# Optimization experiments

Hardware: AMD Instinct MI355X
Metric: run time of the kernel (lower is better)

The kernel has to match this reference:

```python
import jax, jax.numpy as jnp
import numpy as np

N_NODES = 100000
N_EDGES = 1600000
N_FEAT = 16
HEADS = 4


def _feast_conv(x, src, dst, U, c, W, b):
    """FeaStConv: q = softmax_h(u^T(x_j - x_i) + c); out_i = mean_j sum_h q_h * (W_h x_j) + b."""
    n = x.shape[0]
    e = src.shape[0]
    xj = x[src]                                   # [E, Fin] gather
    q = jax.nn.softmax(jnp.matmul(xj - x[dst], U) + c, axis=-1)   # [E, H]
    xs = jnp.matmul(xj, W).reshape(e, HEADS, -1)  # [E, H, Fout]
    msg = jnp.einsum('eh,eho->eo', q, xs)         # [E, Fout]
    deg = jax.ops.segment_sum(jnp.ones((e,), x.dtype), dst, num_segments=n)
    agg = jax.ops.segment_sum(msg, dst, num_segments=n)
    return agg / jnp.maximum(deg, 1.0)[:, None] + b


def setup_inputs() -> dict:
    key = jax.random.key(0)
    ks = jax.random.split(key, 32)
    s = 0.1
    d = {
        'x': jax.random.normal(ks[0], (N_NODES, N_FEAT), jnp.float32),
        'edge_index': jax.random.randint(ks[1], (2, N_EDGES), 0, N_NODES, jnp.int32),
        # conv1: 16 -> 16
        'U1': jax.random.normal(ks[2], (N_FEAT, HEADS), jnp.float32) * s,
        'c1': jnp.zeros((HEADS,), jnp.float32),
        'W1': jax.random.normal(ks[3], (N_FEAT, HEADS * 16), jnp.float32) * s,
        'b1': jnp.zeros((16,), jnp.float32),
        # conv2: 16 -> 32
        'U2': jax.random.normal(ks[4], (16, HEADS), jnp.float32) * s,
        'c2': jnp.zeros((HEADS,), jnp.float32),
        'W2': jax.random.normal(ks[5], (16, HEADS * 32), jnp.float32) * s,
        'b2': jnp.zeros((32,), jnp.float32),
        # conv3: 32 -> 64
        'U3': jax.random.normal(ks[6], (32, HEADS), jnp.float32) * s,
        'c3': jnp.zeros((HEADS,), jnp.float32),
        'W3': jax.random.normal(ks[7], (32, HEADS * 64), jnp.float32) * s,
        'b3': jnp.zeros((64,), jnp.float32),
        # linear tail 64->32->16->8->4->1
        'lw1': jax.random.normal(ks[8], (64, 32), jnp.float32) * s,
        'lb1': jnp.zeros((32,), jnp.float32),
        'lw2': jax.random.normal(ks[9], (32, 16), jnp.float32) * s,
        'lb2': jnp.zeros((16,), jnp.float32),
        'lw3': jax.random.normal(ks[10], (16, 8), jnp.float32) * s,
        'lb3': jnp.zeros((8,), jnp.float32),
        'lw4': jax.random.normal(ks[11], (8, 4), jnp.float32) * s,
        'lb4': jnp.zeros((4,), jnp.float32),
        'lw5': jax.random.normal(ks[12], (4, 1), jnp.float32) * s,
        'lb5': jnp.zeros((1,), jnp.float32),
    }
    return d


def reference(x, edge_index, U1, c1, W1, b1, U2, c2, W2, b2, U3, c3, W3, b3,
              lw1, lb1, lw2, lb2, lw3, lb3, lw4, lb4, lw5, lb5):
    src, dst = edge_index[0], edge_index[1]
    h = jax.nn.relu(_feast_conv(x, src, dst, U1, c1, W1, b1))
    h = jax.nn.relu(_feast_conv(h, src, dst, U2, c2, W2, b2))
    h = jax.nn.relu(_feast_conv(h, src, dst, U3, c3, W3, b3))
    # dropout disabled (inference / drop_bool=False): Linear+ReLU tail
    h = jax.nn.relu(jnp.matmul(h, lw1) + lb1)
    h = jax.nn.relu(jnp.matmul(h, lw2) + lb2)
    h = jax.nn.relu(jnp.matmul(h, lw3) + lb3)
    h = jax.nn.relu(jnp.matmul(h, lw4) + lb4)
    return jax.nn.sigmoid(jnp.matmul(h, lw5) + lb5)   # [N, 1]
```

## Files before the change

kernel.cpp:

```cpp
#include <hip/hip_runtime.h>
#include <math.h>

#define N_NODES 100000
#define N_EDGES 1600000
#define HEADS 4
#define NBKT ((N_NODES + 255) / 256)
#define CHUNK_E 4096
#define NCHUNK ((N_EDGES + CHUNK_E - 1) / CHUNK_E)
#define GN ((N_NODES + 255) / 256)
#define SUM_ROWS 16
#define NRB ((NCHUNK + SUM_ROWS - 1) / SUM_ROWS)

typedef unsigned short ushort_t;
typedef unsigned char  uchar_t;

__device__ __forceinline__ ushort_t f2bf(float x) {
    unsigned u = __float_as_uint(x);
    u += 0x7FFF + ((u >> 16) & 1);
    return (ushort_t)(u >> 16);
}
__device__ __forceinline__ float bf2f(ushort_t v) {
    return __uint_as_float(((unsigned)v) << 16);
}
__device__ __forceinline__ void unpack2(unsigned u, float& lo, float& hi) {
    lo = __uint_as_float(u << 16);
    hi = __uint_as_float(u & 0xffff0000u);
}
__device__ __forceinline__ uchar_t f2fp8(float x) {
    if (x <= 0.0f) return 0;
    unsigned u = __float_as_uint(x) + (1u << 19);
    int e = (int)(u >> 23) - 127 + 15;
    if (e <= 0) return 0;
    if (e > 31) return (uchar_t)255;
    return (uchar_t)((e << 3) | ((u >> 20) & 7));
}
__device__ __forceinline__ float fp8d(uchar_t b) {
    unsigned v = (((unsigned)(b >> 3) + 112u) << 23) | ((unsigned)(b & 7) << 20);
    return (b == 0) ? 0.0f : __uint_as_float(v);
}


__global__ __launch_bounds__(256) void bhist_pcast_kernel(
        const int* __restrict__ dst, int* __restrict__ hist_rows,
        const float* __restrict__ x, const float* __restrict__ U,
        float* __restrict__ p, ushort_t* __restrict__ xbf,
        int* __restrict__ bucket_cnt)
{
    __shared__ int h[NBKT];
    if (blockIdx.x < NCHUNK) {
        for (int i = threadIdx.x; i < NBKT; i += 256) h[i] = 0;
        __syncthreads();
        int base = blockIdx.x * CHUNK_E;
        #pragma unroll
        for (int j = 0; j < CHUNK_E / 256; j++) {
            int e = base + j * 256 + threadIdx.x;
            if (e < N_EDGES) atomicAdd(&h[dst[e] >> 8], 1);
        }
        __syncthreads();
        for (int i = threadIdx.x; i < NBKT; i += 256)
            hist_rows[(size_t)blockIdx.x * NBKT + i] = h[i];
    } else if (blockIdx.x < NCHUNK + GN) {
        int n = (blockIdx.x - NCHUNK) * 256 + threadIdx.x;
        if (n >= N_NODES) return;
        float a0 = 0, a1 = 0, a2 = 0, a3 = 0;
        const float* hr = x + (size_t)n * 16;
        float xv[16];
        #pragma unroll
        for (int f = 0; f < 16; f++) {
            xv[f] = hr[f];
            a0 += xv[f] * U[f * 4 + 0];
            a1 += xv[f] * U[f * 4 + 1];
            a2 += xv[f] * U[f * 4 + 2];
            a3 += xv[f] * U[f * 4 + 3];
        }
        *(float4*)(p + (size_t)n * 4) = make_float4(a0, a1, a2, a3);
        #pragma unroll
        for (int j = 0; j < 4; j++) {
            ushort4 u;
            u.x = f2bf(xv[4 * j + 0]); u.y = f2bf(xv[4 * j + 1]);
            u.z = f2bf(xv[4 * j + 2]); u.w = f2bf(xv[4 * j + 3]);
            *(ushort4*)(xbf + (size_t)n * 16 + 4 * j) = u;
        }
    } else {
        for (int i = threadIdx.x; i < NBKT; i += 256) bucket_cnt[i] = 0;
    }
}


__global__ __launch_bounds__(256) void ksum_kernel(const int* __restrict__ hist_rows,
                                                   int* __restrict__ bucket_cnt) {
    int r0 = blockIdx.x * SUM_ROWS;
    int r1 = min(r0 + SUM_ROWS, NCHUNK);
    for (int i = threadIdx.x; i < NBKT; i += 256) {
        int v = 0;
        for (int r = r0; r < r1; r++) v += hist_rows[(size_t)r * NBKT + i];
        if (v) atomicAdd(&bucket_cnt[i], v);
    }
}


__global__ __launch_bounds__(512) void bscan_kernel(const int* __restrict__ bucket_cnt,
                                                    int* __restrict__ bucket_base,
                                                    int* __restrict__ bucket_cursor) {
    __shared__ int tmp[512];
    int i = threadIdx.x;
    int v = (i < NBKT) ? bucket_cnt[i] : 0;
    tmp[i] = v;
    __syncthreads();
    for (int off = 1; off < 512; off <<= 1) {
        int t = (i >= off) ? tmp[i - off] : 0;
        __syncthreads();
        tmp[i] += t;
        __syncthreads();
    }
    int excl = tmp[i] - v;
    if (i < NBKT) { bucket_base[i] = excl; bucket_cursor[i] = excl; }
    if (i == NBKT) bucket_base[NBKT] = N_EDGES;
}


__global__ __launch_bounds__(256) void partition_kernel(const int* __restrict__ src,
                                                        const int* __restrict__ dst,
                                                        int* __restrict__ bucket_cursor,
                                                        int* __restrict__ csr_tmp) {
    constexpr int EPT = CHUNK_E / 256;
    __shared__ int h[NBKT];
    __shared__ int gbase[NBKT];
    __shared__ int rcnt[NBKT];
    for (int i = threadIdx.x; i < NBKT; i += 256) { h[i] = 0; rcnt[i] = 0; }
    __syncthreads();
    int base = blockIdx.x * CHUNK_E;
    int d[EPT], s[EPT];
    #pragma unroll
    for (int j = 0; j < EPT; j++) {
        int e = base + j * 256 + threadIdx.x;
        d[j] = (e < N_EDGES) ? dst[e] : -1;
        s[j] = (e < N_EDGES) ? src[e] : 0;
        if (d[j] >= 0) atomicAdd(&h[d[j] >> 8], 1);
    }
    __syncthreads();
    for (int i = threadIdx.x; i < NBKT; i += 256)
        if (h[i]) gbase[i] = atomicAdd(&bucket_cursor[i], h[i]);
    __syncthreads();
    #pragma unroll
    for (int j = 0; j < EPT; j++) {
        if (d[j] >= 0) {
            int b = d[j] >> 8;
            int r = atomicAdd(&rcnt[b], 1);
            csr_tmp[gbase[b] + r] = ((d[j] & 255) << 20) | s[j];
        }
    }
}


__global__ __launch_bounds__(256) void bucket_build_kernel(const int* __restrict__ bucket_base,
                                                           const int* __restrict__ csr_tmp,
                                                           int* __restrict__ rowptr,
                                                           int* __restrict__ csr_src) {
    __shared__ int cnt[256];
    __shared__ int tscan[256];
    __shared__ int exc[256];
    __shared__ int stage[8192];
    int b = blockIdx.x;
    int rbeg = bucket_base[b], rend = bucket_base[b + 1];
    int sz = rend - rbeg;
    int tid = threadIdx.x;

    cnt[tid] = 0;
    __syncthreads();
    for (int k = rbeg + tid; k < rend; k += 256) atomicAdd(&cnt[csr_tmp[k] >> 20], 1);
    __syncthreads();
    int v = cnt[tid];
    tscan[tid] = v;
    __syncthreads();
    for (int off = 1; off < 256; off <<= 1) {
        int t = (tid >= off) ? tscan[tid - off] : 0;
        __syncthreads();
        tscan[tid] += t;
        __syncthreads();
    }
    int ex = tscan[tid] - v;
    int node = b * 256 + tid;
    if (node < N_NODES) rowptr[node] = rbeg + ex;
    if (b == 0 && tid == 0) rowptr[N_NODES] = N_EDGES;
    exc[tid] = ex;
    cnt[tid] = 0;
    __syncthreads();

    if (sz <= 8192) {
        for (int k = rbeg + tid; k < rend; k += 256) {
            int pk = csr_tmp[k];
            int dl = pk >> 20;
            int r  = atomicAdd(&cnt[dl], 1);
            stage[exc[dl] + r] = pk;
        }
        __syncthreads();
        for (int i = tid; i < sz; i += 256) csr_src[rbeg + i] = stage[i];
    } else {
        for (int k = rbeg + tid; k < rend; k += 256) {
            int pk = csr_tmp[k];
            int dl = pk >> 20;
            int r  = atomicAdd(&cnt[dl], 1);
            csr_src[rbeg + exc[dl] + r] = pk;
        }
    }
}


template<int FIN, int FOUT, int OUT_FP8>
__global__ __launch_bounds__(256) void conv_fused_kernel(
        const int* __restrict__ rowptr, const int* __restrict__ csr_src,
        const float* __restrict__ p, const float* __restrict__ cvec,
        const ushort_t* __restrict__ hprev,
        const float* __restrict__ W,
        const float* __restrict__ b,
        ushort_t* __restrict__ out_bf,
        uchar_t* __restrict__ out_f8,
        const float* __restrict__ Unext,
        float* __restrict__ pnext)
{
    constexpr int LPN   = FIN / 4;
    constexpr int NPB   = 256 / LPN;
    constexpr int CHUNK = 1024;
    constexpr int K     = 4 * FIN;
    constexpr int ZK    = K + 4;
    constexpr int HS    = FOUT + 1;
    constexpr int WSZ   = K * FOUT;
    constexpr int UNION_A = CHUNK * 16 + CHUNK * 4;
    constexpr int UNION_B = NPB * ZK * 4 + NPB * HS * 4;
    constexpr int UNION   = UNION_A > UNION_B ? UNION_A : UNION_B;

    __shared__ int    sbeg[NPB + 1];
    __shared__ float4 pds[NPB];
    __shared__ float  Ws[WSZ];
    __shared__ float  Uloc[FOUT * 4];
    __shared__ __align__(16) char ubuf[UNION];
    float4* qs    = (float4*)ubuf;
    int*    ssrc  = (int*)(ubuf + CHUNK * 16);
    float*  ztile = (float*)ubuf;
    float*  hout  = (float*)(ubuf + NPB * ZK * 4);

    int tid  = threadIdx.x;
    int nloc = tid / LPN;
    int fl   = (tid - nloc * LPN) * 4;
    int n0   = blockIdx.x * NPB;
    int n    = n0 + nloc;
    int dbase = n0 & 255;

    for (int i = tid; i <= NPB; i += 256) {
        int idx = n0 + i;
        sbeg[i] = rowptr[idx > N_NODES ? N_NODES : idx];
    }
    for (int i = tid; i < NPB; i += 256) {
        int idx = n0 + i;
        pds[i] = *(const float4*)(p + (size_t)(idx < N_NODES ? idx : N_NODES - 1) * 4);
    }
    for (int i = tid; i < WSZ; i += 256) {
        int f = i / (4 * FOUT);
        int r = i - f * (4 * FOUT);
        int h = r / FOUT;
        int o = r - h * FOUT;
        Ws[(h * FIN + f) * FOUT + o] = W[i];
    }
    for (int i = tid; i < FOUT * 4; i += 256) Uloc[i] = Unext[i];
    float c0 = cvec[0], c1 = cvec[1], c2 = cvec[2], c3 = cvec[3];
    __syncthreads();

    int BB = sbeg[0], BE = sbeg[NPB];
    int beg = sbeg[nloc], end = sbeg[nloc + 1];

    float4 acc0 = make_float4(0, 0, 0, 0), acc1 = acc0, acc2 = acc0, acc3 = acc0;

    for (int cbase = BB; cbase < BE; cbase += CHUNK) {
        int cend = min(cbase + CHUNK, BE);
        __syncthreads();
        for (int k = cbase + tid; k < cend; k += 256) {
            int pk = csr_src[k];
            int s  = pk & ((1 << 20) - 1);
            int nl = (pk >> 20) - dbase;
            float4 ps = *(const float4*)(p + (size_t)s * 4);
            float4 pd = pds[nl];
            float l0 = ps.x - pd.x + c0;
            float l1 = ps.y - pd.y + c1;
            float l2 = ps.z - pd.z + c2;
            float l3 = ps.w - pd.w + c3;
            float m  = fmaxf(fmaxf(l0, l1), fmaxf(l2, l3));
            float e0 = __expf(l0 - m), e1 = __expf(l1 - m);
            float e2 = __expf(l2 - m), e3 = __expf(l3 - m);
            float deg = (float)(sbeg[nl + 1] - sbeg[nl]);
            float inv = 1.0f / (fmaxf(deg, 1.0f) * (e0 + e1 + e2 + e3));
            qs[k - cbase]   = make_float4(e0 * inv, e1 * inv, e2 * inv, e3 * inv);
            ssrc[k - cbase] = s;
        }
        __syncthreads();
        int kb = (beg > cbase ? beg : cbase) - cbase;
        int ke = (end < cend ? end : cend) - cbase;
        int k = kb;
        for (; k + 4 <= ke; k += 4) {
            uint2 r[4];
            #pragma unroll
            for (int j = 0; j < 4; j++)
                r[j] = *(const uint2*)(hprev + (size_t)ssrc[k + j] * FIN + fl);
            float xv[4][4];
            #pragma unroll
            for (int j = 0; j < 4; j++) {
                unpack2(r[j].x, xv[j][0], xv[j][1]);
                unpack2(r[j].y, xv[j][2], xv[j][3]);
            }
            #pragma unroll
            for (int j = 0; j < 4; j++) {
                float4 q = qs[k + j];
                acc0.x += q.x * xv[j][0]; acc0.y += q.x * xv[j][1];
                acc0.z += q.x * xv[j][2]; acc0.w += q.x * xv[j][3];
                acc1.x += q.y * xv[j][0]; acc1.y += q.y * xv[j][1];
                acc1.z += q.y * xv[j][2]; acc1.w += q.y * xv[j][3];
                acc2.x += q.z * xv[j][0]; acc2.y += q.z * xv[j][1];
                acc2.z += q.z * xv[j][2]; acc2.w += q.z * xv[j][3];
                acc3.x += q.w * xv[j][0]; acc3.y += q.w * xv[j][1];
                acc3.z += q.w * xv[j][2]; acc3.w += q.w * xv[j][3];
            }
        }
        for (; k < ke; k++) {
            float x0, x1, x2, x3;
            uint2 r = *(const uint2*)(hprev + (size_t)ssrc[k] * FIN + fl);
            unpack2(r.x, x0, x1);
            unpack2(r.y, x2, x3);
            float4 q = qs[k];
            acc0.x += q.x * x0; acc0.y += q.x * x1; acc0.z += q.x * x2; acc0.w += q.x * x3;
            acc1.x += q.y * x0; acc1.y += q.y * x1; acc1.z += q.y * x2; acc1.w += q.y * x3;
            acc2.x += q.z * x0; acc2.y += q.z * x1; acc2.z += q.z * x2; acc2.w += q.z * x3;
            acc3.x += q.w * x0; acc3.y += q.w * x1; acc3.z += q.w * x2; acc3.w += q.w * x3;
        }
    }

    __syncthreads();
    {
        float* zr = ztile + nloc * ZK;
        *(float4*)(zr + 0 * FIN + fl) = acc0;
        *(float4*)(zr + 1 * FIN + fl) = acc1;
        *(float4*)(zr + 2 * FIN + fl) = acc2;
        *(float4*)(zr + 3 * FIN + fl) = acc3;
    }
    __syncthreads();

    constexpr int OQ  = FOUT / 4;
    constexpr int QPT = (NPB * OQ) / 256;
    #pragma unroll
    for (int rq = 0; rq < QPT; rq++) {
        int idx = tid + 256 * rq;
        int j   = idx / OQ;
        int o4  = idx - j * OQ;
        float4 acc = *(const float4*)(b + 4 * o4);
        const float* zr = ztile + j * ZK;
        #pragma unroll 4
        for (int kq = 0; kq < K / 4; kq++) {
            float4 zt = *(const float4*)(zr + 4 * kq);
            #pragma unroll
            for (int jj = 0; jj < 4; jj++) {
                float4 wv = *(const float4*)(Ws + (4 * kq + jj) * FOUT + 4 * o4);
                float s = (&zt.x)[jj];
                acc.x += s * wv.x;
                acc.y += s * wv.y;
                acc.z += s * wv.z;
                acc.w += s * wv.w;
            }
        }
        acc.x = fmaxf(acc.x, 0.0f);
        acc.y = fmaxf(acc.y, 0.0f);
        acc.z = fmaxf(acc.z, 0.0f);
        acc.w = fmaxf(acc.w, 0.0f);
        float* hr = hout + j * HS + 4 * o4;
        hr[0] = acc.x; hr[1] = acc.y; hr[2] = acc.z; hr[3] = acc.w;
        int nn = n0 + j;
        if (nn < N_NODES) {
            if (OUT_FP8) {
                unsigned pk = (unsigned)f2fp8(acc.x) | ((unsigned)f2fp8(acc.y) << 8) |
                              ((unsigned)f2fp8(acc.z) << 16) | ((unsigned)f2fp8(acc.w) << 24);
                *(unsigned*)(out_f8 + (size_t)nn * FOUT + 4 * o4) = pk;
            } else {
                ushort4 u;
                u.x = f2bf(acc.x); u.y = f2bf(acc.y); u.z = f2bf(acc.z); u.w = f2bf(acc.w);
                *(ushort4*)(out_bf + (size_t)nn * FOUT + 4 * o4) = u;
            }
        }
    }

    __syncthreads();
    if (tid < NPB) {
        int nn = n0 + tid;
        if (nn < N_NODES) {
            float a0 = 0, a1 = 0, a2 = 0, a3 = 0;
            const float* hr = hout + tid * HS;
            #pragma unroll
            for (int ff = 0; ff < FOUT; ff++) {
                float xv = hr[ff];
                a0 += xv * Uloc[ff * 4 + 0];
                a1 += xv * Uloc[ff * 4 + 1];
                a2 += xv * Uloc[ff * 4 + 2];
                a3 += xv * Uloc[ff * 4 + 3];
            }
            *(float4*)(pnext + (size_t)nn * 4) = make_float4(a0, a1, a2, a3);
        }
    }
}


template<int FIN>
__global__ __launch_bounds__(256) void zgather_kernel(
        const int* __restrict__ rowptr, const int* __restrict__ csr_src,
        const float* __restrict__ p, const float* __restrict__ cvec,
        const uchar_t* __restrict__ hf8,
        ushort_t* __restrict__ z)
{
    constexpr int LPN   = FIN / 4;
    constexpr int NPB   = 256 / LPN;
    constexpr int CHUNK = 1024;
    __shared__ int    sbeg[NPB + 1];
    __shared__ float4 pds[NPB];
    __shared__ float4 qs[CHUNK];
    __shared__ int    ssrc[CHUNK];

    int tid  = threadIdx.x;
    int nloc = tid / LPN;
    int fl   = (tid - nloc * LPN) * 4;
    int n0   = blockIdx.x * NPB;
    int n    = n0 + nloc;
    int dbase = n0 & 255;

    for (int i = tid; i <= NPB; i += 256) {
        int idx = n0 + i;
        sbeg[i] = rowptr[idx > N_NODES ? N_NODES : idx];
    }
    for (int i = tid; i < NPB; i += 256) {
        int idx = n0 + i;
        pds[i] = *(const float4*)(p + (size_t)(idx < N_NODES ? idx : N_NODES - 1) * 4);
    }
    float c0 = cvec[0], c1 = cvec[1], c2 = cvec[2], c3 = cvec[3];
    __syncthreads();

    int BB = sbeg[0], BE = sbeg[NPB];
    int beg = sbeg[nloc], end = sbeg[nloc + 1];

    float4 acc0 = make_float4(0, 0, 0, 0), acc1 = acc0, acc2 = acc0, acc3 = acc0;

    for (int cbase = BB; cbase < BE; cbase += CHUNK) {
        int cend = min(cbase + CHUNK, BE);
        __syncthreads();
        for (int k = cbase + tid; k < cend; k += 256) {
            int pk = csr_src[k];
            int s  = pk & ((1 << 20) - 1);
            int nl = (pk >> 20) - dbase;
            float4 ps = *(const float4*)(p + (size_t)s * 4);
            float4 pd = pds[nl];
            float l0 = ps.x - pd.x + c0;
            float l1 = ps.y - pd.y + c1;
            float l2 = ps.z - pd.z + c2;
            float l3 = ps.w - pd.w + c3;
            float m  = fmaxf(fmaxf(l0, l1), fmaxf(l2, l3));
            float e0 = __expf(l0 - m), e1 = __expf(l1 - m);
            float e2 = __expf(l2 - m), e3 = __expf(l3 - m);
            float deg = (float)(sbeg[nl + 1] - sbeg[nl]);
            float inv = 1.0f / (fmaxf(deg, 1.0f) * (e0 + e1 + e2 + e3));
            qs[k - cbase]   = make_float4(e0 * inv, e1 * inv, e2 * inv, e3 * inv);
            ssrc[k - cbase] = s;
        }
        __syncthreads();
        int kb = (beg > cbase ? beg : cbase) - cbase;
        int ke = (end < cend ? end : cend) - cbase;
        int k = kb;
        for (; k + 4 <= ke; k += 4) {
            unsigned r[4];
            #pragma unroll
            for (int j = 0; j < 4; j++)
                r[j] = *(const unsigned*)(hf8 + (size_t)ssrc[k + j] * FIN + fl);
            float xv[4][4];
            #pragma unroll
            for (int j = 0; j < 4; j++) {
                xv[j][0] = fp8d((uchar_t)(r[j] & 255));
                xv[j][1] = fp8d((uchar_t)((r[j] >> 8) & 255));
                xv[j][2] = fp8d((uchar_t)((r[j] >> 16) & 255));
                xv[j][3] = fp8d((uchar_t)(r[j] >> 24));
            }
            #pragma unroll
            for (int j = 0; j < 4; j++) {
                float4 q = qs[k + j];
                acc0.x += q.x * xv[j][0]; acc0.y += q.x * xv[j][1];
                acc0.z += q.x * xv[j][2]; acc0.w += q.x * xv[j][3];
                acc1.x += q.y * xv[j][0]; acc1.y += q.y * xv[j][1];
                acc1.z += q.y * xv[j][2]; acc1.w += q.y * xv[j][3];
                acc2.x += q.z * xv[j][0]; acc2.y += q.z * xv[j][1];
                acc2.z += q.z * xv[j][2]; acc2.w += q.z * xv[j][3];
                acc3.x += q.w * xv[j][0]; acc3.y += q.w * xv[j][1];
                acc3.z += q.w * xv[j][2]; acc3.w += q.w * xv[j][3];
            }
        }
        for (; k < ke; k++) {
            unsigned r = *(const unsigned*)(hf8 + (size_t)ssrc[k] * FIN + fl);
            float x0 = fp8d((uchar_t)(r & 255));
            float x1 = fp8d((uchar_t)((r >> 8) & 255));
            float x2 = fp8d((uchar_t)((r >> 16) & 255));
            float x3 = fp8d((uchar_t)(r >> 24));
            float4 q = qs[k];
            acc0.x += q.x * x0; acc0.y += q.x * x1; acc0.z += q.x * x2; acc0.w += q.x * x3;
            acc1.x += q.y * x0; acc1.y += q.y * x1; acc1.z += q.y * x2; acc1.w += q.y * x3;
            acc2.x += q.z * x0; acc2.y += q.z * x1; acc2.z += q.z * x2; acc2.w += q.z * x3;
            acc3.x += q.w * x0; acc3.y += q.w * x1; acc3.z += q.w * x2; acc3.w += q.w * x3;
        }
    }

    if (n < N_NODES) {
        size_t base = (size_t)n * (4 * FIN) + fl;
        ushort4 u;
        u.x = f2bf(acc0.x); u.y = f2bf(acc0.y); u.z = f2bf(acc0.z); u.w = f2bf(acc0.w);
        *(ushort4*)(z + base) = u;
        u.x = f2bf(acc1.x); u.y = f2bf(acc1.y); u.z = f2bf(acc1.z); u.w = f2bf(acc1.w);
        *(ushort4*)(z + base + FIN) = u;
        u.x = f2bf(acc2.x); u.y = f2bf(acc2.y); u.z = f2bf(acc2.z); u.w = f2bf(acc2.w);
        *(ushort4*)(z + base + 2 * FIN) = u;
        u.x = f2bf(acc3.x); u.y = f2bf(acc3.y); u.z = f2bf(acc3.z); u.w = f2bf(acc3.w);
        *(ushort4*)(z + base + 3 * FIN) = u;
    }
}


template<int FIN, int FOUT>
__global__ __launch_bounds__(256, 4) void post_kernel(
        const ushort_t* __restrict__ z,
        const float* __restrict__ W,
        const float* __restrict__ b,
        ushort_t* __restrict__ out_bf)
{
    constexpr int K   = 4 * FIN;
    constexpr int OL  = FOUT / 4;
    constexpr int NPB = 4 * (256 / OL);
    constexpr int WSZ = FIN * 4 * FOUT;
    __shared__ float Wp[WSZ];
    for (int i = threadIdx.x; i < WSZ; i += 256) {
        int f = i / (4 * FOUT);
        int r = i - f * (4 * FOUT);
        int h = r / FOUT;
        int o = r - h * FOUT;
        Wp[(h * FIN + f) * FOUT + o] = W[i];
    }
    __syncthreads();

    int ol = threadIdx.x % OL;
    int g  = threadIdx.x / OL;
    int n0 = blockIdx.x * NPB + g * 4;

    float4 bv = *(const float4*)(b + 4 * ol);
    float4 acc[4];
    const ushort_t* zr[4];
    #pragma unroll
    for (int j = 0; j < 4; j++) {
        acc[j] = make_float4(0.f, 0.f, 0.f, 0.f);
        int nn = n0 + j; if (nn > N_NODES - 1) nn = N_NODES - 1;
        zr[j] = z + (size_t)nn * K;
    }

    #pragma unroll 2
    for (int kq = 0; kq < K / 4; kq++) {
        float zv[4][4];
        #pragma unroll
        for (int j = 0; j < 4; j++) {
            ushort4 zu = *(const ushort4*)(zr[j] + 4 * kq);
            zv[j][0] = bf2f(zu.x); zv[j][1] = bf2f(zu.y);
            zv[j][2] = bf2f(zu.z); zv[j][3] = bf2f(zu.w);
        }
        #pragma unroll
        for (int jj = 0; jj < 4; jj++) {
            float4 wv = *(const float4*)(Wp + (4 * kq + jj) * FOUT + 4 * ol);
            #pragma unroll
            for (int j = 0; j < 4; j++) {
                float s = zv[j][jj];
                acc[j].x += s * wv.x;
                acc[j].y += s * wv.y;
                acc[j].z += s * wv.z;
                acc[j].w += s * wv.w;
            }
        }
    }

    #pragma unroll
    for (int j = 0; j < 4; j++) {
        int nn = n0 + j;
        if (nn < N_NODES) {
            ushort4 u;
            u.x = f2bf(fmaxf(acc[j].x + bv.x, 0.0f));
            u.y = f2bf(fmaxf(acc[j].y + bv.y, 0.0f));
            u.z = f2bf(fmaxf(acc[j].z + bv.z, 0.0f));
            u.w = f2bf(fmaxf(acc[j].w + bv.w, 0.0f));
            *(ushort4*)(out_bf + (size_t)nn * FOUT + 4 * ol) = u;
        }
    }
}


__global__ __launch_bounds__(256) void tail_kernel(
        const ushort_t* __restrict__ h,
        const float* __restrict__ lw1, const float* __restrict__ lb1,
        const float* __restrict__ lw2, const float* __restrict__ lb2,
        const float* __restrict__ lw3, const float* __restrict__ lb3,
        const float* __restrict__ lw4, const float* __restrict__ lb4,
        const float* __restrict__ lw5, const float* __restrict__ lb5,
        float* __restrict__ out)
{
    __shared__ float w1[64 * 32], w2[32 * 16], w3[16 * 8], w4[8 * 4], w5[4];
    __shared__ float B1[32], B2[16], B3[8], B4[4], B5[1];
    for (int i = threadIdx.x; i < 64 * 32; i += blockDim.x) w1[i] = lw1[i];
    for (int i = threadIdx.x; i < 32 * 16; i += blockDim.x) w2[i] = lw2[i];
    for (int i = threadIdx.x; i < 16 * 8;  i += blockDim.x) w3[i] = lw3[i];
    for (int i = threadIdx.x; i < 8 * 4;   i += blockDim.x) w4[i] = lw4[i];
    for (int i = threadIdx.x; i < 4;       i += blockDim.x) w5[i] = lw5[i];
    for (int i = threadIdx.x; i < 32; i += blockDim.x) B1[i] = lb1[i];
    for (int i = threadIdx.x; i < 16; i += blockDim.x) B2[i] = lb2[i];
    for (int i = threadIdx.x; i < 8;  i += blockDim.x) B3[i] = lb3[i];
    for (int i = threadIdx.x; i < 4;  i += blockDim.x) B4[i] = lb4[i];
    if (threadIdx.x == 0) B5[0] = lb5[0];
    __syncthreads();

    int n = blockIdx.x * blockDim.x + threadIdx.x;
    if (n >= N_NODES) return;

    float a[64];
    const uint4* hrow = (const uint4*)(h + (size_t)n * 64);
    #pragma unroll
    for (int j = 0; j < 8; j++) {
        uint4 v = hrow[j];
        unpack2(v.x, a[8 * j + 0], a[8 * j + 1]);
        unpack2(v.y, a[8 * j + 2], a[8 * j + 3]);
        unpack2(v.z, a[8 * j + 4], a[8 * j + 5]);
        unpack2(v.w, a[8 * j + 6], a[8 * j + 7]);
    }

    float t1[32];
    for (int o = 0; o < 32; o++) {
        float acc = B1[o];
        #pragma unroll
        for (int i = 0; i < 64; i++) acc += a[i] * w1[i * 32 + o];
        t1[o] = fmaxf(acc, 0.0f);
    }
    float t2[16];
    for (int o = 0; o < 16; o++) {
        float acc = B2[o];
        #pragma unroll
        for (int i = 0; i < 32; i++) acc += t1[i] * w2[i * 16 + o];
        t2[o] = fmaxf(acc, 0.0f);
    }
    float t3[8];
    for (int o = 0; o < 8; o++) {
        float acc = B3[o];
        #pragma unroll
        for (int i = 0; i < 16; i++) acc += t2[i] * w3[i * 8 + o];
        t3[o] = fmaxf(acc, 0.0f);
    }
    float t4[4];
    for (int o = 0; o < 4; o++) {
        float acc = B4[o];
        #pragma unroll
        for (int i = 0; i < 8; i++) acc += t3[i] * w4[i * 4 + o];
        t4[o] = fmaxf(acc, 0.0f);
    }
    float zf = B5[0];
    #pragma unroll
    for (int i = 0; i < 4; i++) zf += t4[i] * w5[i];
    out[n] = 1.0f / (1.0f + expf(-zf));
}


extern "C" void kernel_launch(void* const* d_in, const int* in_sizes, int n_in,
                              void* d_out, int out_size, void* d_ws, size_t ws_size,
                              hipStream_t stream) {
    const float* x   = (const float*)d_in[0];
    const int*   ei  = (const int*)d_in[1];
    const int*   src = ei;
    const int*   dst = ei + N_EDGES;
    const float* U1 = (const float*)d_in[2];  const float* c1 = (const float*)d_in[3];
    const float* W1 = (const float*)d_in[4];  const float* b1 = (const float*)d_in[5];
    const float* U2 = (const float*)d_in[6];  const float* c2 = (const float*)d_in[7];
    const float* W2 = (const float*)d_in[8];  const float* b2 = (const float*)d_in[9];
    const float* U3 = (const float*)d_in[10]; const float* c3 = (const float*)d_in[11];
    const float* W3 = (const float*)d_in[12]; const float* b3 = (const float*)d_in[13];
    const float* lw1 = (const float*)d_in[14]; const float* lb1 = (const float*)d_in[15];
    const float* lw2 = (const float*)d_in[16]; const float* lb2 = (const float*)d_in[17];
    const float* lw3 = (const float*)d_in[18]; const float* lb3 = (const float*)d_in[19];
    const float* lw4 = (const float*)d_in[20]; const float* lb4 = (const float*)d_in[21];
    const float* lw5 = (const float*)d_in[22]; const float* lb5 = (const float*)d_in[23];

    char* ws = (char*)d_ws;
    size_t off = 0;
    auto alloc = [&](size_t bytes) -> void* {
        void* ptr = (void*)(ws + off);
        off += (bytes + 255) & ~(size_t)255;
        return ptr;
    };
    int*      hist_rows     = (int*)alloc((size_t)NCHUNK * NBKT * 4);
    int*      bucket_cnt    = (int*)alloc((size_t)(NBKT + 1) * 4);
    int*      bucket_base   = (int*)alloc((size_t)(NBKT + 1) * 4);
    int*      bucket_cursor = (int*)alloc((size_t)NBKT * 4);
    int*      csr_tmp       = (int*)alloc((size_t)N_EDGES * 4);
    int*      rowptr        = (int*)alloc(((size_t)N_NODES + 1) * 4);
    int*      csr_src       = (int*)alloc((size_t)N_EDGES * 4);
    float*    p             = (float*)alloc((size_t)N_NODES * 4 * 4);
    ushort_t* z             = (ushort_t*)alloc((size_t)N_NODES * 128 * 2);
    ushort_t* xbf           = (ushort_t*)alloc((size_t)N_NODES * 16 * 2);
    ushort_t* h1bf          = (ushort_t*)alloc((size_t)N_NODES * 16 * 2);
    uchar_t*  h2f8          = (uchar_t*)alloc((size_t)N_NODES * 32);
    ushort_t* h3bf          = (ushort_t*)alloc((size_t)N_NODES * 64 * 2);
    (void)ws_size;

    const int B = 256;

    bhist_pcast_kernel<<<NCHUNK + GN + 1, B, 0, stream>>>(dst, hist_rows, x, U1, p, xbf,
                                                          bucket_cnt);
    ksum_kernel<<<NRB, B, 0, stream>>>(hist_rows, bucket_cnt);
    bscan_kernel<<<1, 512, 0, stream>>>(bucket_cnt, bucket_base, bucket_cursor);
    partition_kernel<<<NCHUNK, B, 0, stream>>>(src, dst, bucket_cursor, csr_tmp);
    bucket_build_kernel<<<NBKT, B, 0, stream>>>(bucket_base, csr_tmp, rowptr, csr_src);

    const int ZG16 = (N_NODES + 63) / 64;
    const int ZG32 = (N_NODES + 31) / 32;
    const int NPB3 = 4 * (256 / (64 / 4));

    conv_fused_kernel<16, 16, 0><<<ZG16, B, 0, stream>>>(
        rowptr, csr_src, p, c1, xbf, W1, b1, h1bf, nullptr, U2, p);

    conv_fused_kernel<16, 32, 1><<<ZG16, B, 0, stream>>>(
        rowptr, csr_src, p, c2, h1bf, W2, b2, nullptr, h2f8, U3, p);

    zgather_kernel<32><<<ZG32, B, 0, stream>>>(rowptr, csr_src, p, c3, h2f8, z);
    post_kernel<32, 64><<<(N_NODES + NPB3 - 1) / NPB3, B, 0, stream>>>(z, W3, b3, h3bf);
    tail_kernel<<<GN, B, 0, stream>>>(h3bf, lw1, lb1, lw2, lb2, lw3, lb3,
                                      lw4, lb4, lw5, lb5, (float*)d_out);
}
```

Before: 321.8 us.

## Recompute attention logits per edge inline instead of staging softmax weights in shared memory

The fused conv kernel used to stage each chunk's softmax weights and source indices in shared memory, reading per-source projections p[s]. Each edge's logit is now computed directly from the gathered features using U held in registers, reduced across the 4 lanes of a node with xor-shuffles, and the node's loop walks its own CSR range with no block syncs. This removes the shared staging buffer and the per-chunk barriers, and shrinks shared memory. The cost is redundant dot-product and exp work per lane, plus separate p buffers (aliased onto z and h3bf) so a layer does not overwrite the projections it is still reading.

```diff
diff --git a/kernel.cpp b/kernel.cpp
--- a/kernel.cpp
+++ b/kernel.cpp
@@ -211,6 +211,7 @@
 __global__ __launch_bounds__(256) void conv_fused_kernel(
         const int* __restrict__ rowptr, const int* __restrict__ csr_src,
         const float* __restrict__ p, const float* __restrict__ cvec,
+        const float* __restrict__ Ucur,
         const ushort_t* __restrict__ hprev,
         const float* __restrict__ W,
         const float* __restrict__ b,
@@ -221,22 +222,17 @@
 {
     constexpr int LPN   = FIN / 4;
     constexpr int NPB   = 256 / LPN;
-    constexpr int CHUNK = 1024;
     constexpr int K     = 4 * FIN;
     constexpr int ZK    = K + 4;
     constexpr int HS    = FOUT + 1;
     constexpr int WSZ   = K * FOUT;
-    constexpr int UNION_A = CHUNK * 16 + CHUNK * 4;
-    constexpr int UNION_B = NPB * ZK * 4 + NPB * HS * 4;
-    constexpr int UNION   = UNION_A > UNION_B ? UNION_A : UNION_B;
+    constexpr int UBYTES = NPB * ZK * 4 + NPB * HS * 4;
 
     __shared__ int    sbeg[NPB + 1];
-    __shared__ float4 pds[NPB];
-    __shared__ float  Ws[WSZ];
+    __shared__ __align__(16) float4 pds[NPB];
+    __shared__ __align__(16) float  Ws[WSZ];
     __shared__ float  Uloc[FOUT * 4];
-    __shared__ __align__(16) char ubuf[UNION];
-    float4* qs    = (float4*)ubuf;
-    int*    ssrc  = (int*)(ubuf + CHUNK * 16);
+    __shared__ __align__(16) char ubuf[UBYTES];
     float*  ztile = (float*)ubuf;
     float*  hout  = (float*)(ubuf + NPB * ZK * 4);
 
@@ -244,8 +240,6 @@
     int nloc = tid / LPN;
     int fl   = (tid - nloc * LPN) * 4;
     int n0   = blockIdx.x * NPB;
-    int n    = n0 + nloc;
-    int dbase = n0 & 255;
 
     for (int i = tid; i <= NPB; i += 256) {
         int idx = n0 + i;
@@ -264,76 +258,60 @@
     }
     for (int i = tid; i < FOUT * 4; i += 256) Uloc[i] = Unext[i];
     float c0 = cvec[0], c1 = cvec[1], c2 = cvec[2], c3 = cvec[3];
-    __syncthreads();
-
-    int BB = sbeg[0], BE = sbeg[NPB];
+    float4 u0 = *(const float4*)(Ucur + (fl + 0) * 4);
+    float4 u1 = *(const float4*)(Ucur + (fl + 1) * 4);
+    float4 u2 = *(const float4*)(Ucur + (fl + 2) * 4);
+    float4 u3 = *(const float4*)(Ucur + (fl + 3) * 4);
+    __syncthreads();
+
     int beg = sbeg[nloc], end = sbeg[nloc + 1];
+    float invdeg = 1.0f / fmaxf((float)(end - beg), 1.0f);
+    float4 pd = pds[nloc];
 
     float4 acc0 = make_float4(0, 0, 0, 0), acc1 = acc0, acc2 = acc0, acc3 = acc0;
 
-    for (int cbase = BB; cbase < BE; cbase += CHUNK) {
-        int cend = min(cbase + CHUNK, BE);
-        __syncthreads();
-        for (int k = cbase + tid; k < cend; k += 256) {
-            int pk = csr_src[k];
-            int s  = pk & ((1 << 20) - 1);
-            int nl = (pk >> 20) - dbase;
-            float4 ps = *(const float4*)(p + (size_t)s * 4);
-            float4 pd = pds[nl];
-            float l0 = ps.x - pd.x + c0;
-            float l1 = ps.y - pd.y + c1;
-            float l2 = ps.z - pd.z + c2;
-            float l3 = ps.w - pd.w + c3;
-            float m  = fmaxf(fmaxf(l0, l1), fmaxf(l2, l3));
-            float e0 = __expf(l0 - m), e1 = __expf(l1 - m);
-            float e2 = __expf(l2 - m), e3 = __expf(l3 - m);
-            float deg = (float)(sbeg[nl + 1] - sbeg[nl]);
-            float inv = 1.0f / (fmaxf(deg, 1.0f) * (e0 + e1 + e2 + e3));
-            qs[k - cbase]   = make_float4(e0 * inv, e1 * inv, e2 * inv, e3 * inv);
-            ssrc[k - cbase] = s;
-        }
-        __syncthreads();
-        int kb = (beg > cbase ? beg : cbase) - cbase;
-        int ke = (end < cend ? end : cend) - cbase;
-        int k = kb;
-        for (; k + 4 <= ke; k += 4) {
-            uint2 r[4];
-            #pragma unroll
-            for (int j = 0; j < 4; j++)
-                r[j] = *(const uint2*)(hprev + (size_t)ssrc[k + j] * FIN + fl);
-            float xv[4][4];
-            #pragma unroll
-            for (int j = 0; j < 4; j++) {
-                unpack2(r[j].x, xv[j][0], xv[j][1]);
-                unpack2(r[j].y, xv[j][2], xv[j][3]);
-            }
-            #pragma unroll
-            for (int j = 0; j < 4; j++) {
-                float4 q = qs[k + j];
-                acc0.x += q.x * xv[j][0]; acc0.y += q.x * xv[j][1];
-                acc0.z += q.x * xv[j][2]; acc0.w += q.x * xv[j][3];
-                acc1.x += q.y * xv[j][0]; acc1.y += q.y * xv[j][1];
-                acc1.z += q.y * xv[j][2]; acc1.w += q.y * xv[j][3];
-                acc2.x += q.z * xv[j][0]; acc2.y += q.z * xv[j][1];
-                acc2.z += q.z * xv[j][2]; acc2.w += q.z * xv[j][3];
-                acc3.x += q.w * xv[j][0]; acc3.y += q.w * xv[j][1];
-                acc3.z += q.w * xv[j][2]; acc3.w += q.w * xv[j][3];
-            }
-        }
-        for (; k < ke; k++) {
-            float x0, x1, x2, x3;
-            uint2 r = *(const uint2*)(hprev + (size_t)ssrc[k] * FIN + fl);
-            unpack2(r.x, x0, x1);
-            unpack2(r.y, x2, x3);
-            float4 q = qs[k];
-            acc0.x += q.x * x0; acc0.y += q.x * x1; acc0.z += q.x * x2; acc0.w += q.x * x3;
-            acc1.x += q.y * x0; acc1.y += q.y * x1; acc1.z += q.y * x2; acc1.w += q.y * x3;
-            acc2.x += q.z * x0; acc2.y += q.z * x1; acc2.z += q.z * x2; acc2.w += q.z * x3;
-            acc3.x += q.w * x0; acc3.y += q.w * x1; acc3.z += q.w * x2; acc3.w += q.w * x3;
-        }
-    }
-
-    __syncthreads();
+    auto edge = [&](uint2 r) {
+        float x0, x1, x2, x3;
+        unpack2(r.x, x0, x1);
+        unpack2(r.y, x2, x3);
+        float t0 = x0 * u0.x + x1 * u1.x + x2 * u2.x + x3 * u3.x;
+        float t1 = x0 * u0.y + x1 * u1.y + x2 * u2.y + x3 * u3.y;
+        float t2 = x0 * u0.z + x1 * u1.z + x2 * u2.z + x3 * u3.z;
+        float t3 = x0 * u0.w + x1 * u1.w + x2 * u2.w + x3 * u3.w;
+        t0 += __shfl_xor(t0, 1); t0 += __shfl_xor(t0, 2);
+        t1 += __shfl_xor(t1, 1); t1 += __shfl_xor(t1, 2);
+        t2 += __shfl_xor(t2, 1); t2 += __shfl_xor(t2, 2);
+        t3 += __shfl_xor(t3, 1); t3 += __shfl_xor(t3, 2);
+        float l0 = t0 - pd.x + c0;
+        float l1 = t1 - pd.y + c1;
+        float l2 = t2 - pd.z + c2;
+        float l3 = t3 - pd.w + c3;
+        float m  = fmaxf(fmaxf(l0, l1), fmaxf(l2, l3));
+        float e0 = __expf(l0 - m), e1 = __expf(l1 - m);
+        float e2 = __expf(l2 - m), e3 = __expf(l3 - m);
+        float inv = invdeg / (e0 + e1 + e2 + e3);
+        float q0 = e0 * inv, q1 = e1 * inv, q2 = e2 * inv, q3 = e3 * inv;
+        acc0.x += q0 * x0; acc0.y += q0 * x1; acc0.z += q0 * x2; acc0.w += q0 * x3;
+        acc1.x += q1 * x0; acc1.y += q1 * x1; acc1.z += q1 * x2; acc1.w += q1 * x3;
+        acc2.x += q2 * x0; acc2.y += q2 * x1; acc2.z += q2 * x2; acc2.w += q2 * x3;
+        acc3.x += q3 * x0; acc3.y += q3 * x1; acc3.z += q3 * x2; acc3.w += q3 * x3;
+    };
+
+    int k = beg;
+    for (; k + 2 <= end; k += 2) {
+        int s0 = csr_src[k]     & ((1 << 20) - 1);
+        int s1 = csr_src[k + 1] & ((1 << 20) - 1);
+        uint2 r0 = *(const uint2*)(hprev + (size_t)s0 * FIN + fl);
+        uint2 r1 = *(const uint2*)(hprev + (size_t)s1 * FIN + fl);
+        edge(r0);
+        edge(r1);
+    }
+    if (k < end) {
+        int s0 = csr_src[k] & ((1 << 20) - 1);
+        uint2 r0 = *(const uint2*)(hprev + (size_t)s0 * FIN + fl);
+        edge(r0);
+    }
+
     {
         float* zr = ztile + nloc * ZK;
         *(float4*)(zr + 0 * FIN + fl) = acc0;
@@ -416,8 +394,8 @@
     constexpr int NPB   = 256 / LPN;
     constexpr int CHUNK = 1024;
     __shared__ int    sbeg[NPB + 1];
-    __shared__ float4 pds[NPB];
-    __shared__ float4 qs[CHUNK];
+    __shared__ __align__(16) float4 pds[NPB];
+    __shared__ __align__(16) float4 qs[CHUNK];
     __shared__ int    ssrc[CHUNK];
 
     int tid  = threadIdx.x;
@@ -534,7 +512,7 @@
     constexpr int OL  = FOUT / 4;
     constexpr int NPB = 4 * (256 / OL);
     constexpr int WSZ = FIN * 4 * FOUT;
-    __shared__ float Wp[WSZ];
+    __shared__ __align__(16) float Wp[WSZ];
     for (int i = threadIdx.x; i < WSZ; i += 256) {
         int f = i / (4 * FOUT);
         int r = i - f * (4 * FOUT);
@@ -605,7 +583,8 @@
         const float* __restrict__ lw5, const float* __restrict__ lb5,
         float* __restrict__ out)
 {
-    __shared__ float w1[64 * 32], w2[32 * 16], w3[16 * 8], w4[8 * 4], w5[4];
+    __shared__ __align__(16) float w1[64 * 32];
+    __shared__ float w2[32 * 16], w3[16 * 8], w4[8 * 4], w5[4];
     __shared__ float B1[32], B2[16], B3[8], B4[4], B5[1];
     for (int i = threadIdx.x; i < 64 * 32; i += blockDim.x) w1[i] = lw1[i];
     for (int i = threadIdx.x; i < 32 * 16; i += blockDim.x) w2[i] = lw2[i];
@@ -708,6 +687,8 @@
     uchar_t*  h2f8          = (uchar_t*)alloc((size_t)N_NODES * 32);
     ushort_t* h3bf          = (ushort_t*)alloc((size_t)N_NODES * 64 * 2);
     (void)ws_size;
+    float* p2 = (float*)z;
+    float* p3 = (float*)h3bf;
 
     const int B = 256;
 
@@ -723,12 +704,12 @@
     const int NPB3 = 4 * (256 / (64 / 4));
 
     conv_fused_kernel<16, 16, 0><<<ZG16, B, 0, stream>>>(
-        rowptr, csr_src, p, c1, xbf, W1, b1, h1bf, nullptr, U2, p);
+        rowptr, csr_src, p, c1, U1, xbf, W1, b1, h1bf, nullptr, U2, p2);
 
     conv_fused_kernel<16, 32, 1><<<ZG16, B, 0, stream>>>(
-        rowptr, csr_src, p, c2, h1bf, W2, b2, nullptr, h2f8, U3, p);
-
-    zgather_kernel<32><<<ZG32, B, 0, stream>>>(rowptr, csr_src, p, c3, h2f8, z);
+        rowptr, csr_src, p2, c2, U2, h1bf, W2, b2, nullptr, h2f8, U3, p3);
+
+    zgather_kernel<32><<<ZG32, B, 0, stream>>>(rowptr, csr_src, p3, c3, h2f8, z);
     post_kernel<32, 64><<<(N_NODES + NPB3 - 1) / NPB3, B, 0, stream>>>(z, W3, b3, h3bf);
     tail_kernel<<<GN, B, 0, stream>>>(h3bf, lw1, lb1, lw2, lb2, lw3, lb3,
                                       lw4, lb4, lw5, lb5, (float*)d_out);
```

Measured after the change: 333.8 us. 3.7% more time.
